# Performance work log

Measured on AMD Instinct MI355X. Metric: run time of the kernel, lower is better.

## Reference

```python
import jax, jax.numpy as jnp
import numpy as np

ROUTER_TEMP = 1.0
ALPHA = 1.0
EPS = 1e-6


def _rmsnorm(x, w):
    var = jnp.mean(x * x, axis=-1, keepdims=True)
    return x * jax.lax.rsqrt(var + EPS) * w


def _block(x, wg, wu, wd, nw):
    # stand-in recursion block: residual RMSNorm + SwiGLU MLP (pointwise over tokens)
    xn = _rmsnorm(x, nw)
    return x + (jax.nn.silu(xn @ wg) * (xn @ wu)) @ wd


def setup_inputs() -> dict:
    key = jax.random.key(0)
    ks = jax.random.split(key, 5)
    B, S, D, F, L = 2, 4096, 2048, 8192, 2
    return {
        "hidden_states": jax.random.normal(ks[0], (B, S, D), jnp.float32),
        "router_w": jax.random.normal(ks[1], (L, D), jnp.float32) * 0.02,
        "Wg": jax.random.normal(ks[2], (L, D, F), jnp.float32) * (D ** -0.5),
        "Wu": jax.random.normal(ks[3], (L, D, F), jnp.float32) * (D ** -0.5),
        "Wd": jax.random.normal(ks[4], (L, F, D), jnp.float32) * (F ** -0.5),
        "norm_w": jnp.ones((L, D), jnp.float32),
    }


def reference(hidden_states, router_w, Wg, Wu, Wd, norm_w):
    L = router_w.shape[0]
    # router: logits (B,S,L), softmax probs scaled by alpha, top-1 routing
    router_logits = (hidden_states / ROUTER_TEMP) @ router_w.T
    router_probs = jax.nn.softmax(router_logits, axis=-1) * ALPHA
    idx = jnp.argmax(router_probs, axis=-1)                      # (B,S)
    weights = jnp.take_along_axis(router_probs, idx[..., None], axis=-1)  # (B,S,1)
    # run every level's block densely on all tokens (pointwise blocks =>
    # identical math to original gather/pad/compute/scatter), then select
    y = jax.vmap(_block, in_axes=(None, 0, 0, 0, 0))(hidden_states, Wg, Wu, Wd, norm_w)  # (L,B,S,D)
    onehot = jax.nn.one_hot(idx, L, dtype=hidden_states.dtype)   # (B,S,L)
    sel = jnp.einsum("lbsd,bsl->bsd", y, onehot)
    output = hidden_states + weights * sel                       # gating == 'weighted'
    # router z-loss: mean of squared logsumexp over levels
    z = jax.nn.logsumexp(router_logits, axis=-1)
    router_z_loss = jnp.mean(z * z)
    return output, router_z_loss
```

## Files before the change

kernel.cpp:

```cpp
#include <hip/hip_runtime.h>
#include <hip/hip_bf16.h>
#include <stdint.h>

#define B_    2
#define S_    4096
#define D_    2048
#define F_    8192
#define L_    2
#define FQ    (F_ / 4)
#define NTOK  (B_ * S_)
#define RCAP  (NTOK + 128)
#define EPS_  1e-6f

typedef __attribute__((ext_vector_type(8))) short s16x8;
typedef __attribute__((ext_vector_type(4))) float f32x4;

typedef unsigned short u16;
typedef unsigned int   u32;

#define OFF_CNT   ((size_t)0)
#define OFF_ZL    ((size_t)128)
#define OFF_MAP   ((size_t)384)
#define OFF_WROW  ((size_t)33664)
#define OFF_WTOK  ((size_t)66944)
#define OFF_XG    ((size_t)99712)
#define OFF_HQ    ((size_t)34178432)
#define OFF_WA    ((size_t)68257152)
#define OFF_WB    ((size_t)85034368)

__device__ __forceinline__ u16 f2bf(float f) {
    u32 u = __builtin_bit_cast(u32, f);
    u += 0x7fff + ((u >> 16) & 1);
    return (u16)(u >> 16);
}

__device__ __forceinline__ void gl16(const u16* g, u16* l) {
    __builtin_amdgcn_global_load_lds(
        (const __attribute__((address_space(1))) void*)g,
        (__attribute__((address_space(3))) void*)l, 16, 0, 0);
}

__global__ void k_init(int* counts, float* zacc) {
    if (threadIdx.x == 0) { counts[0] = 0; counts[16] = 0; }
    zacc[threadIdx.x & 63] = 0.f;
}

__global__ __launch_bounds__(256) void k_router(
    const float* __restrict__ hs, const float* __restrict__ rw,
    const float* __restrict__ nw, int* __restrict__ counts,
    float* __restrict__ zacc, int* __restrict__ tmap,
    float* __restrict__ wrow, float* __restrict__ wtok, u16* __restrict__ Xg)
{
    int t = blockIdx.x;
    int tid = threadIdx.x;
    const float* x = hs + (size_t)t * D_;
    float xs[8];
    float sxx = 0.f, s0 = 0.f, s1 = 0.f;
#pragma unroll
    for (int i = 0; i < 8; i++) {
        int d = tid + i * 256;
        float v = x[d];
        xs[i] = v;
        sxx += v * v;
        s0  += v * rw[d];
        s1  += v * rw[D_ + d];
    }
#pragma unroll
    for (int off = 32; off; off >>= 1) {
        sxx += __shfl_down(sxx, off, 64);
        s0  += __shfl_down(s0,  off, 64);
        s1  += __shfl_down(s1,  off, 64);
    }
    __shared__ float red[3][4];
    __shared__ float bcf[1];
    __shared__ int   bci[2];
    int wave = tid >> 6, lane = tid & 63;
    if (lane == 0) { red[0][wave] = sxx; red[1][wave] = s0; red[2][wave] = s1; }
    __syncthreads();
    if (tid == 0) {
        sxx = red[0][0] + red[0][1] + red[0][2] + red[0][3];
        s0  = red[1][0] + red[1][1] + red[1][2] + red[1][3];
        s1  = red[2][0] + red[2][1] + red[2][2] + red[2][3];
        float m  = fmaxf(s0, s1);
        float e0 = __expf(s0 - m), e1 = __expf(s1 - m);
        float Z  = e0 + e1;
        int   idx = (s1 > s0) ? 1 : 0;
        float p   = ((idx == 0) ? e0 : e1) / Z;
        float z   = m + __logf(Z);
        atomicAdd(&zacc[t & 63], z * z * (1.0f / NTOK));
        int pos = atomicAdd(&counts[idx << 4], 1);
        int row = (idx == 0) ? pos : (RCAP - 1 - pos);
        tmap[row] = t;
        wrow[row] = p;
        wtok[t]   = p;
        bcf[0] = rsqrtf(sxx * (1.0f / D_) + EPS_);
        bci[0] = idx; bci[1] = row;
    }
    __syncthreads();
    float inv = bcf[0];
    int idx = bci[0], row = bci[1];
    u16* xr = Xg + (size_t)row * D_;
    const float* w = nw + (size_t)idx * D_;
#pragma unroll
    for (int i = 0; i < 8; i++) {
        int d = tid + i * 256;
        xr[d] = f2bf(xs[i] * inv * w[d]);
    }
}

__global__ __launch_bounds__(256) void k_gap(const int* counts, int* tmap, u16* Xg) {
    int row = counts[0] + blockIdx.x;
    uint4* p = (uint4*)(Xg + (size_t)row * D_);
    p[threadIdx.x] = make_uint4(0u, 0u, 0u, 0u);
    if (threadIdx.x == 0) tmap[row] = -1;
}

__global__ __launch_bounds__(256) void k_outinit(
    const float* __restrict__ hs, const float* __restrict__ wtok,
    float* __restrict__ out)
{
    int t = blockIdx.x;
    float c = 1.f + wtok[t];
    const float4* ip = (const float4*)(hs + (size_t)t * D_);
    float4* op = (float4*)(out + (size_t)t * D_);
#pragma unroll
    for (int i = 0; i < 2; i++) {
        float4 v = ip[threadIdx.x + i * 256];
        v.x *= c; v.y *= c; v.z *= c; v.w *= c;
        op[threadIdx.x + i * 256] = v;
    }
}

__global__ __launch_bounds__(256) void k_transpose(
    const float* __restrict__ in, u16* __restrict__ out,
    int R, int C, int r0, int c0, int RL, int CL)
{
    __shared__ float tile[32][33];
    int lc0 = blockIdx.x * 32;
    int lr0 = blockIdx.y * 32;
    const float* ip = in + (size_t)blockIdx.z * (size_t)R * (size_t)C;
    u16* op = out + (size_t)blockIdx.z * (size_t)CL * (size_t)RL;
    int tx = threadIdx.x & 31, ty = threadIdx.x >> 5;
#pragma unroll
    for (int i = 0; i < 4; i++)
        tile[ty + i * 8][tx] = ip[(size_t)(r0 + lr0 + ty + i * 8) * C + (c0 + lc0 + tx)];
    __syncthreads();
#pragma unroll
    for (int i = 0; i < 4; i++)
        op[(size_t)(lc0 + ty + i * 8) * RL + lr0 + tx] = f2bf(tile[tx][ty + i * 8]);
}

__global__ __launch_bounds__(256, 2) void k_gemm1(
    const u16* __restrict__ Xg, const u16* __restrict__ WgT,
    const u16* __restrict__ WuT, const int* __restrict__ counts,
    u16* __restrict__ Hq)
{
    int nt = blockIdx.x, mt = blockIdx.y;
    int count0 = counts[0];
    int level = (mt * 128 < count0) ? 0 : 1;
    const u16* Bg = WgT + (size_t)level * FQ * D_;
    const u16* Bu = WuT + (size_t)level * FQ * D_;

    __shared__ __align__(16) u16 As[128 * 32], Bgs[64 * 32], Bus[64 * 32];

    int tid = threadIdx.x, lane = tid & 63, wave = tid >> 6;
    int wm = wave >> 1, wn = wave & 1;
    int quad = lane >> 4, ln = lane & 15;

    f32x4 accG[4][2] = {}, accU[4][2] = {};

    const u16* ga = Xg + (size_t)(mt * 128 + (tid >> 2)) * D_ + (tid & 3) * 8;
    const u16* gg = Bg + (size_t)(nt * 64 + (tid >> 2)) * D_ + (tid & 3) * 8;
    const u16* gu = Bu + (size_t)(nt * 64 + (tid >> 2)) * D_ + (tid & 3) * 8;

    u16* lA = As  + (size_t)wave * 512;
    u16* lG = Bgs + (size_t)wave * 512;
    u16* lU = Bus + (size_t)wave * 512;

    for (int k0 = 0; k0 < D_; k0 += 32) {
        __syncthreads();
        gl16(ga + k0, lA);
        gl16(ga + (size_t)64 * D_ + k0, lA + 2048);
        gl16(gg + k0, lG);
        gl16(gu + k0, lU);
        __syncthreads();
        s16x8 a[4], bg[2], bu[2];
#pragma unroll
        for (int i = 0; i < 4; i++)
            a[i]  = *(const s16x8*)(As  + (wm * 64 + i * 16 + ln) * 32 + quad * 8);
#pragma unroll
        for (int j = 0; j < 2; j++) {
            bg[j] = *(const s16x8*)(Bgs + (wn * 32 + j * 16 + ln) * 32 + quad * 8);
            bu[j] = *(const s16x8*)(Bus + (wn * 32 + j * 16 + ln) * 32 + quad * 8);
        }
#pragma unroll
        for (int mi = 0; mi < 4; mi++)
#pragma unroll
            for (int ni = 0; ni < 2; ni++) {
                accG[mi][ni] = __builtin_amdgcn_mfma_f32_16x16x32_bf16(a[mi], bg[ni], accG[mi][ni], 0, 0, 0);
                accU[mi][ni] = __builtin_amdgcn_mfma_f32_16x16x32_bf16(a[mi], bu[ni], accU[mi][ni], 0, 0, 0);
            }
    }

    int rowbase = mt * 128 + wm * 64;
    int colbase = nt * 64 + wn * 32;
#pragma unroll
    for (int mi = 0; mi < 4; mi++)
#pragma unroll
        for (int ni = 0; ni < 2; ni++)
#pragma unroll
            for (int r = 0; r < 4; r++) {
                float g = accG[mi][ni][r], u = accU[mi][ni][r];
                float h = g / (1.f + __expf(-g)) * u;
                int row = rowbase + mi * 16 + quad * 4 + r;
                int col = colbase + ni * 16 + ln;
                Hq[(size_t)row * FQ + col] = f2bf(h);
            }
}

__global__ __launch_bounds__(256, 2) void k_gemm2(
    const u16* __restrict__ Hq, const u16* __restrict__ WdT,
    const int* __restrict__ counts, const int* __restrict__ tmap,
    const float* __restrict__ wrow, float* __restrict__ out)
{
    int nt = blockIdx.x, mt = blockIdx.y;
    int count0 = counts[0];
    int level = (mt * 128 < count0) ? 0 : 1;
    const u16* Bd = WdT + (size_t)level * D_ * FQ;

    __shared__ __align__(16) u16 As[128 * 32], Bs[128 * 32];
    __shared__ int   stok[128];
    __shared__ float sw[128];

    int tid = threadIdx.x, lane = tid & 63, wave = tid >> 6;
    int wm = wave >> 1, wn = wave & 1;
    int quad = lane >> 4, ln = lane & 15;

    if (tid < 128) { stok[tid] = tmap[mt * 128 + tid]; sw[tid] = wrow[mt * 128 + tid]; }

    f32x4 acc[4][4] = {};

    const u16* ga = Hq + (size_t)(mt * 128 + (tid >> 2)) * FQ + (tid & 3) * 8;
    const u16* gb = Bd + (size_t)(nt * 128 + (tid >> 2)) * FQ + (tid & 3) * 8;

    u16* lA = As + (size_t)wave * 512;
    u16* lB = Bs + (size_t)wave * 512;

    for (int k0 = 0; k0 < FQ; k0 += 32) {
        __syncthreads();
        gl16(ga + k0, lA);
        gl16(ga + (size_t)64 * FQ + k0, lA + 2048);
        gl16(gb + k0, lB);
        gl16(gb + (size_t)64 * FQ + k0, lB + 2048);
        __syncthreads();
        s16x8 a[4], b[4];
#pragma unroll
        for (int i = 0; i < 4; i++) {
            a[i] = *(const s16x8*)(As + (wm * 64 + i * 16 + ln) * 32 + quad * 8);
            b[i] = *(const s16x8*)(Bs + (wn * 64 + i * 16 + ln) * 32 + quad * 8);
        }
#pragma unroll
        for (int mi = 0; mi < 4; mi++)
#pragma unroll
            for (int ni = 0; ni < 4; ni++)
                acc[mi][ni] = __builtin_amdgcn_mfma_f32_16x16x32_bf16(a[mi], b[ni], acc[mi][ni], 0, 0, 0);
    }

    int colbase = nt * 128 + wn * 64;
#pragma unroll
    for (int mi = 0; mi < 4; mi++)
#pragma unroll
        for (int ni = 0; ni < 4; ni++)
#pragma unroll
            for (int r = 0; r < 4; r++) {
                int rl = wm * 64 + mi * 16 + quad * 4 + r;
                int tok = stok[rl];
                if (tok < 0) continue;
                float w = sw[rl];
                int col = colbase + ni * 16 + ln;
                size_t oidx = (size_t)tok * D_ + col;
                out[oidx] += w * acc[mi][ni][r];
            }
}

__global__ void k_zout(const float* zacc, float* out) {
    float s = 0.f;
#pragma unroll
    for (int i = 0; i < 64; i++) s += zacc[i];
    out[(size_t)NTOK * D_] = s;
}

extern "C" void kernel_launch(void* const* d_in, const int* in_sizes, int n_in,
                              void* d_out, int out_size, void* d_ws, size_t ws_size,
                              hipStream_t stream) {
    const float* hs = (const float*)d_in[0];
    const float* rw = (const float*)d_in[1];
    const float* Wg = (const float*)d_in[2];
    const float* Wu = (const float*)d_in[3];
    const float* Wd = (const float*)d_in[4];
    const float* nw = (const float*)d_in[5];
    float* out = (float*)d_out;

    char* ws = (char*)d_ws;
    int*   counts = (int*)(ws + OFF_CNT);
    float* zacc   = (float*)(ws + OFF_ZL);
    int*   tmap   = (int*)(ws + OFF_MAP);
    float* wrow   = (float*)(ws + OFF_WROW);
    float* wtok   = (float*)(ws + OFF_WTOK);
    u16*   Xg     = (u16*)(ws + OFF_XG);
    u16*   Hq     = (u16*)(ws + OFF_HQ);
    u16*   WA     = (u16*)(ws + OFF_WA);
    u16*   WB     = (u16*)(ws + OFF_WB);

    k_init<<<1, 64, 0, stream>>>(counts, zacc);
    k_router<<<NTOK, 256, 0, stream>>>(hs, rw, nw, counts, zacc, tmap, wrow, wtok, Xg);
    k_gap<<<128, 256, 0, stream>>>(counts, tmap, Xg);
    k_outinit<<<NTOK, 256, 0, stream>>>(hs, wtok, out);

    for (int q = 0; q < 4; q++) {
        k_transpose<<<dim3(FQ / 32, D_ / 32, L_), 256, 0, stream>>>(Wg, WA, D_, F_, 0, q * FQ, D_, FQ);
        k_transpose<<<dim3(FQ / 32, D_ / 32, L_), 256, 0, stream>>>(Wu, WB, D_, F_, 0, q * FQ, D_, FQ);
        k_gemm1<<<dim3(FQ / 64, RCAP / 128), 256, 0, stream>>>(Xg, WA, WB, counts, Hq);
        k_transpose<<<dim3(D_ / 32, FQ / 32, L_), 256, 0, stream>>>(Wd, WA, F_, D_, q * FQ, 0, FQ, D_);
        k_gemm2<<<dim3(D_ / 128, RCAP / 128), 256, 0, stream>>>(Hq, WA, counts, tmap, wrow, out);
    }
    k_zout<<<1, 1, 0, stream>>>(zacc, out);
}
```

Before: 1.830 ms.

## Pipeline GEMMs with multi-buffered LDS, larger tiles and swizzled loads

Both GEMM kernels move to 512-thread blocks with 256-wide N tiles. Global-to-LDS loads go into a 3-stage (gemm1) or 4-stage (gemm2) ring buffer, using manual vmcnt waits and raw barriers instead of two __syncthreads per K step. An XOR swizzle on the LDS layout reduces bank conflicts, and s_setprio raises wave priority around the MFMA blocks. This is meant to hide global load latency and cut sync overhead, at the cost of much more LDS per block, which lowers occupancy, and of fragile hand-written waitcnt logic.

```diff
diff --git a/kernel.cpp b/kernel.cpp
--- a/kernel.cpp
+++ b/kernel.cpp
@@ -39,6 +39,8 @@
         (const __attribute__((address_space(1))) void*)g,
         (__attribute__((address_space(3))) void*)l, 16, 0, 0);
 }
+
+#define MF(acc, va, vb) acc = __builtin_amdgcn_mfma_f32_16x16x32_bf16(va, vb, acc, 0, 0, 0)
 
 __global__ void k_init(int* counts, float* zacc) {
     if (threadIdx.x == 0) { counts[0] = 0; counts[16] = 0; }
@@ -150,7 +152,7 @@
         op[(size_t)(lc0 + ty + i * 8) * RL + lr0 + tx] = f2bf(tile[tx][ty + i * 8]);
 }
 
-__global__ __launch_bounds__(256, 2) void k_gemm1(
+__global__ __launch_bounds__(512, 2) void k_gemm1(
     const u16* __restrict__ Xg, const u16* __restrict__ WgT,
     const u16* __restrict__ WuT, const int* __restrict__ counts,
     u16* __restrict__ Hq)
@@ -161,64 +163,115 @@
     const u16* Bg = WgT + (size_t)level * FQ * D_;
     const u16* Bu = WuT + (size_t)level * FQ * D_;
 
-    __shared__ __align__(16) u16 As[128 * 32], Bgs[64 * 32], Bus[64 * 32];
+    __shared__ __align__(16) u16 lds[3 * 20480];
 
     int tid = threadIdx.x, lane = tid & 63, wave = tid >> 6;
-    int wm = wave >> 1, wn = wave & 1;
+    int wm = wave >> 2, wn = wave & 3;
     int quad = lane >> 4, ln = lane & 15;
 
-    f32x4 accG[4][2] = {}, accU[4][2] = {};
-
-    const u16* ga = Xg + (size_t)(mt * 128 + (tid >> 2)) * D_ + (tid & 3) * 8;
-    const u16* gg = Bg + (size_t)(nt * 64 + (tid >> 2)) * D_ + (tid & 3) * 8;
-    const u16* gu = Bu + (size_t)(nt * 64 + (tid >> 2)) * D_ + (tid & 3) * 8;
-
-    u16* lA = As  + (size_t)wave * 512;
-    u16* lG = Bgs + (size_t)wave * 512;
-    u16* lU = Bus + (size_t)wave * 512;
-
-    for (int k0 = 0; k0 < D_; k0 += 32) {
-        __syncthreads();
-        gl16(ga + k0, lA);
-        gl16(ga + (size_t)64 * D_ + k0, lA + 2048);
-        gl16(gg + k0, lG);
-        gl16(gu + k0, lU);
-        __syncthreads();
+    int srow = tid >> 2;
+    int sswz = ((tid & 3) ^ (srow & 3)) * 8;
+    const u16* gA  = Xg + (size_t)(mt * 128 + srow) * D_ + sswz;
+    const u16* gG0 = Bg + (size_t)(nt * 256 + srow) * D_ + sswz;
+    const u16* gG1 = gG0 + (size_t)128 * D_;
+    const u16* gU0 = Bu + (size_t)(nt * 256 + srow) * D_ + sswz;
+    const u16* gU1 = gU0 + (size_t)128 * D_;
+
+    u16* wd = lds + wave * 512;
+
+    f32x4 accG[4][4] = {}, accU[4][4] = {};
+
+#pragma unroll
+    for (int p = 0; p < 2; ++p) {
+        u16* b = wd + p * 20480;
+        gl16(gA  + p * 32, b);
+        gl16(gG0 + p * 32, b + 4096);
+        gl16(gG1 + p * 32, b + 8192);
+        gl16(gU0 + p * 32, b + 12288);
+        gl16(gU1 + p * 32, b + 16384);
+    }
+    asm volatile("s_waitcnt vmcnt(5)" ::: "memory");
+    asm volatile("s_barrier" ::: "memory");
+
+    int fswz = (quad ^ (ln & 3)) * 8;
+    int aoff = (wm * 64 + ln) * 32 + fswz;
+    int boff = (wn * 64 + ln) * 32 + fswz;
+
+    int cur = 0;
+    for (int t = 0; t < 64; ++t) {
+        const u16* As = lds + cur * 20480;
+        const u16* Gs = As + 4096;
+        const u16* Us = As + 12288;
+        int stg = cur + 2; if (stg >= 3) stg -= 3;
+        u16* sb = lds + stg * 20480 + wave * 512;
+        int koff = (t + 2) * 32;
+        bool do_stage = (t + 2) < 64;
+
         s16x8 a[4], bg[2], bu[2];
 #pragma unroll
-        for (int i = 0; i < 4; i++)
-            a[i]  = *(const s16x8*)(As  + (wm * 64 + i * 16 + ln) * 32 + quad * 8);
-#pragma unroll
-        for (int j = 0; j < 2; j++) {
-            bg[j] = *(const s16x8*)(Bgs + (wn * 32 + j * 16 + ln) * 32 + quad * 8);
-            bu[j] = *(const s16x8*)(Bus + (wn * 32 + j * 16 + ln) * 32 + quad * 8);
-        }
-#pragma unroll
-        for (int mi = 0; mi < 4; mi++)
-#pragma unroll
-            for (int ni = 0; ni < 2; ni++) {
-                accG[mi][ni] = __builtin_amdgcn_mfma_f32_16x16x32_bf16(a[mi], bg[ni], accG[mi][ni], 0, 0, 0);
-                accU[mi][ni] = __builtin_amdgcn_mfma_f32_16x16x32_bf16(a[mi], bu[ni], accU[mi][ni], 0, 0, 0);
+        for (int i = 0; i < 4; ++i) a[i] = *(const s16x8*)(As + i * 512 + aoff);
+#pragma unroll
+        for (int j = 0; j < 2; ++j) {
+            bg[j] = *(const s16x8*)(Gs + j * 512 + boff);
+            bu[j] = *(const s16x8*)(Us + j * 512 + boff);
+        }
+        if (do_stage) {
+            gl16(gA  + koff, sb);
+            gl16(gG0 + koff, sb + 4096);
+            gl16(gG1 + koff, sb + 8192);
+        }
+        __builtin_amdgcn_s_setprio(1);
+#pragma unroll
+        for (int mi = 0; mi < 4; ++mi)
+#pragma unroll
+            for (int j = 0; j < 2; ++j) {
+                MF(accG[mi][j], a[mi], bg[j]);
+                MF(accU[mi][j], a[mi], bu[j]);
             }
+        __builtin_amdgcn_s_setprio(0);
+        asm volatile("s_barrier" ::: "memory");
+
+#pragma unroll
+        for (int j = 0; j < 2; ++j) {
+            bg[j] = *(const s16x8*)(Gs + (2 + j) * 512 + boff);
+            bu[j] = *(const s16x8*)(Us + (2 + j) * 512 + boff);
+        }
+        if (do_stage) {
+            gl16(gU0 + koff, sb + 12288);
+            gl16(gU1 + koff, sb + 16384);
+        }
+        __builtin_amdgcn_s_setprio(1);
+#pragma unroll
+        for (int mi = 0; mi < 4; ++mi)
+#pragma unroll
+            for (int j = 0; j < 2; ++j) {
+                MF(accG[mi][2 + j], a[mi], bg[j]);
+                MF(accU[mi][2 + j], a[mi], bu[j]);
+            }
+        __builtin_amdgcn_s_setprio(0);
+        if (t < 62)       { asm volatile("s_waitcnt vmcnt(5)" ::: "memory"); }
+        else if (t == 62) { asm volatile("s_waitcnt vmcnt(0)" ::: "memory"); }
+        asm volatile("s_barrier" ::: "memory");
+        cur = (cur == 2) ? 0 : cur + 1;
     }
 
     int rowbase = mt * 128 + wm * 64;
-    int colbase = nt * 64 + wn * 32;
-#pragma unroll
-    for (int mi = 0; mi < 4; mi++)
-#pragma unroll
-        for (int ni = 0; ni < 2; ni++)
-#pragma unroll
-            for (int r = 0; r < 4; r++) {
-                float g = accG[mi][ni][r], u = accU[mi][ni][r];
+    int colbase = nt * 256 + wn * 64;
+#pragma unroll
+    for (int mi = 0; mi < 4; ++mi)
+#pragma unroll
+        for (int nj = 0; nj < 4; ++nj)
+#pragma unroll
+            for (int r = 0; r < 4; ++r) {
+                float g = accG[mi][nj][r], u = accU[mi][nj][r];
                 float h = g / (1.f + __expf(-g)) * u;
                 int row = rowbase + mi * 16 + quad * 4 + r;
-                int col = colbase + ni * 16 + ln;
+                int col = colbase + nj * 16 + ln;
                 Hq[(size_t)row * FQ + col] = f2bf(h);
             }
 }
 
-__global__ __launch_bounds__(256, 2) void k_gemm2(
+__global__ __launch_bounds__(512, 2) void k_gemm2(
     const u16* __restrict__ Hq, const u16* __restrict__ WdT,
     const int* __restrict__ counts, const int* __restrict__ tmap,
     const float* __restrict__ wrow, float* __restrict__ out)
@@ -228,58 +281,85 @@
     int level = (mt * 128 < count0) ? 0 : 1;
     const u16* Bd = WdT + (size_t)level * D_ * FQ;
 
-    __shared__ __align__(16) u16 As[128 * 32], Bs[128 * 32];
+    __shared__ __align__(16) u16 lds[4 * 12288];
     __shared__ int   stok[128];
     __shared__ float sw[128];
 
     int tid = threadIdx.x, lane = tid & 63, wave = tid >> 6;
-    int wm = wave >> 1, wn = wave & 1;
+    int wm = wave >> 2, wn = wave & 3;
     int quad = lane >> 4, ln = lane & 15;
 
     if (tid < 128) { stok[tid] = tmap[mt * 128 + tid]; sw[tid] = wrow[mt * 128 + tid]; }
 
+    int srow = tid >> 2;
+    int sswz = ((tid & 3) ^ (srow & 3)) * 8;
+    const u16* gA  = Hq + (size_t)(mt * 128 + srow) * FQ + sswz;
+    const u16* gB0 = Bd + (size_t)(nt * 256 + srow) * FQ + sswz;
+    const u16* gB1 = gB0 + (size_t)128 * FQ;
+
+    u16* wd = lds + wave * 512;
+
     f32x4 acc[4][4] = {};
 
-    const u16* ga = Hq + (size_t)(mt * 128 + (tid >> 2)) * FQ + (tid & 3) * 8;
-    const u16* gb = Bd + (size_t)(nt * 128 + (tid >> 2)) * FQ + (tid & 3) * 8;
-
-    u16* lA = As + (size_t)wave * 512;
-    u16* lB = Bs + (size_t)wave * 512;
-
-    for (int k0 = 0; k0 < FQ; k0 += 32) {
-        __syncthreads();
-        gl16(ga + k0, lA);
-        gl16(ga + (size_t)64 * FQ + k0, lA + 2048);
-        gl16(gb + k0, lB);
-        gl16(gb + (size_t)64 * FQ + k0, lB + 2048);
-        __syncthreads();
+#pragma unroll
+    for (int p = 0; p < 3; ++p) {
+        u16* b = wd + p * 12288;
+        gl16(gA  + p * 32, b);
+        gl16(gB0 + p * 32, b + 4096);
+        gl16(gB1 + p * 32, b + 8192);
+    }
+    asm volatile("s_waitcnt vmcnt(6)" ::: "memory");
+    asm volatile("s_barrier" ::: "memory");
+
+    int fswz = (quad ^ (ln & 3)) * 8;
+    int aoff = (wm * 64 + ln) * 32 + fswz;
+    int boff = (wn * 64 + ln) * 32 + fswz;
+
+    int cur = 0;
+    for (int t = 0; t < 64; ++t) {
+        const u16* As = lds + cur * 12288;
+        const u16* Bs = As + 4096;
+        int stg = cur + 3; if (stg >= 4) stg -= 4;
+        u16* sb = lds + stg * 12288 + wave * 512;
+        int koff = (t + 3) * 32;
+
         s16x8 a[4], b[4];
 #pragma unroll
-        for (int i = 0; i < 4; i++) {
-            a[i] = *(const s16x8*)(As + (wm * 64 + i * 16 + ln) * 32 + quad * 8);
-            b[i] = *(const s16x8*)(Bs + (wn * 64 + i * 16 + ln) * 32 + quad * 8);
-        }
-#pragma unroll
-        for (int mi = 0; mi < 4; mi++)
-#pragma unroll
-            for (int ni = 0; ni < 4; ni++)
-                acc[mi][ni] = __builtin_amdgcn_mfma_f32_16x16x32_bf16(a[mi], b[ni], acc[mi][ni], 0, 0, 0);
-    }
-
-    int colbase = nt * 128 + wn * 64;
-#pragma unroll
-    for (int mi = 0; mi < 4; mi++)
-#pragma unroll
-        for (int ni = 0; ni < 4; ni++)
-#pragma unroll
-            for (int r = 0; r < 4; r++) {
+        for (int i = 0; i < 4; ++i) {
+            a[i] = *(const s16x8*)(As + i * 512 + aoff);
+            b[i] = *(const s16x8*)(Bs + i * 512 + boff);
+        }
+        if (t + 3 < 64) {
+            gl16(gA  + koff, sb);
+            gl16(gB0 + koff, sb + 4096);
+            gl16(gB1 + koff, sb + 8192);
+        }
+        __builtin_amdgcn_s_setprio(1);
+#pragma unroll
+        for (int mi = 0; mi < 4; ++mi)
+#pragma unroll
+            for (int nj = 0; nj < 4; ++nj)
+                MF(acc[mi][nj], a[mi], b[nj]);
+        __builtin_amdgcn_s_setprio(0);
+        if (t < 61)       { asm volatile("s_waitcnt vmcnt(6)" ::: "memory"); }
+        else if (t == 61) { asm volatile("s_waitcnt vmcnt(3)" ::: "memory"); }
+        else if (t == 62) { asm volatile("s_waitcnt vmcnt(0)" ::: "memory"); }
+        asm volatile("s_barrier" ::: "memory");
+        cur = (cur == 3) ? 0 : cur + 1;
+    }
+
+    int colbase = nt * 256 + wn * 64;
+#pragma unroll
+    for (int mi = 0; mi < 4; ++mi)
+#pragma unroll
+        for (int nj = 0; nj < 4; ++nj)
+#pragma unroll
+            for (int r = 0; r < 4; ++r) {
                 int rl = wm * 64 + mi * 16 + quad * 4 + r;
                 int tok = stok[rl];
                 if (tok < 0) continue;
-                float w = sw[rl];
-                int col = colbase + ni * 16 + ln;
-                size_t oidx = (size_t)tok * D_ + col;
-                out[oidx] += w * acc[mi][ni][r];
+                int col = colbase + nj * 16 + ln;
+                out[(size_t)tok * D_ + col] += sw[rl] * acc[mi][nj][r];
             }
 }
 
@@ -320,9 +400,9 @@
     for (int q = 0; q < 4; q++) {
         k_transpose<<<dim3(FQ / 32, D_ / 32, L_), 256, 0, stream>>>(Wg, WA, D_, F_, 0, q * FQ, D_, FQ);
         k_transpose<<<dim3(FQ / 32, D_ / 32, L_), 256, 0, stream>>>(Wu, WB, D_, F_, 0, q * FQ, D_, FQ);
-        k_gemm1<<<dim3(FQ / 64, RCAP / 128), 256, 0, stream>>>(Xg, WA, WB, counts, Hq);
+        k_gemm1<<<dim3(FQ / 256, RCAP / 128), 512, 0, stream>>>(Xg, WA, WB, counts, Hq);
         k_transpose<<<dim3(D_ / 32, FQ / 32, L_), 256, 0, stream>>>(Wd, WA, F_, D_, q * FQ, 0, FQ, D_);
-        k_gemm2<<<dim3(D_ / 128, RCAP / 128), 256, 0, stream>>>(Hq, WA, counts, tmap, wrow, out);
+        k_gemm2<<<dim3(D_ / 256, RCAP / 128), 512, 0, stream>>>(Hq, WA, counts, tmap, wrow, out);
     }
     k_zout<<<1, 1, 0, stream>>>(zacc, out);
 }
```

New measurement: 1.886 ms. 1.03x slower.

## Widen GEMM K-step to 64 with XOR-swizzled LDS and merge Wg/Wu transposes

Applied to the files above, without the earlier changes.

Both GEMM kernels now stage 64-wide K slices into LDS with an XOR swizzle on the 16-byte chunks, which halves the number of barrier pairs and is meant to avoid LDS bank conflicts on the fragment reads. gemm2 uses a smaller 128x64 output tile with fewer accumulators, and both kernels raise launch-bounds occupancy to 3 blocks. The separate Wg and Wu transposes are merged into one launch. LDS arrays are padded, apparently to limit occupancy. The narrower gemm2 tile reuses each A tile less and reads Hq more times.

```diff
diff --git a/kernel.cpp b/kernel.cpp
--- a/kernel.cpp
+++ b/kernel.cpp
@@ -39,6 +39,8 @@
         (const __attribute__((address_space(1))) void*)g,
         (__attribute__((address_space(3))) void*)l, 16, 0, 0);
 }
+
+#define MF(acc, va, vb) acc = __builtin_amdgcn_mfma_f32_16x16x32_bf16(va, vb, acc, 0, 0, 0)
 
 __global__ void k_init(int* counts, float* zacc) {
     if (threadIdx.x == 0) { counts[0] = 0; counts[16] = 0; }
@@ -131,6 +133,27 @@
     }
 }
 
+__global__ __launch_bounds__(256) void k_transposeGU(
+    const float* __restrict__ Wg, const float* __restrict__ Wu,
+    u16* __restrict__ WA, u16* __restrict__ WB, int c0)
+{
+    __shared__ float tile[32][33];
+    int z = blockIdx.z;
+    int m = z & 1, lvl = z >> 1;
+    const float* ip = (m ? Wu : Wg) + (size_t)lvl * D_ * F_;
+    u16* op = (m ? WB : WA) + (size_t)lvl * FQ * D_;
+    int lc0 = blockIdx.x * 32;
+    int lr0 = blockIdx.y * 32;
+    int tx = threadIdx.x & 31, ty = threadIdx.x >> 5;
+#pragma unroll
+    for (int i = 0; i < 4; i++)
+        tile[ty + i * 8][tx] = ip[(size_t)(lr0 + ty + i * 8) * F_ + (c0 + lc0 + tx)];
+    __syncthreads();
+#pragma unroll
+    for (int i = 0; i < 4; i++)
+        op[(size_t)(lc0 + ty + i * 8) * D_ + lr0 + tx] = f2bf(tile[tx][ty + i * 8]);
+}
+
 __global__ __launch_bounds__(256) void k_transpose(
     const float* __restrict__ in, u16* __restrict__ out,
     int R, int C, int r0, int c0, int RL, int CL)
@@ -150,7 +173,7 @@
         op[(size_t)(lc0 + ty + i * 8) * RL + lr0 + tx] = f2bf(tile[tx][ty + i * 8]);
 }
 
-__global__ __launch_bounds__(256, 2) void k_gemm1(
+__global__ __launch_bounds__(256, 3) void k_gemm1(
     const u16* __restrict__ Xg, const u16* __restrict__ WgT,
     const u16* __restrict__ WuT, const int* __restrict__ counts,
     u16* __restrict__ Hq)
@@ -161,64 +184,75 @@
     const u16* Bg = WgT + (size_t)level * FQ * D_;
     const u16* Bu = WuT + (size_t)level * FQ * D_;
 
-    __shared__ __align__(16) u16 As[128 * 32], Bgs[64 * 32], Bus[64 * 32];
+    __shared__ __align__(16) u16 As[8192 + 6144];
+    __shared__ __align__(16) u16 Gs[4096], Us[4096];
 
     int tid = threadIdx.x, lane = tid & 63, wave = tid >> 6;
     int wm = wave >> 1, wn = wave & 1;
     int quad = lane >> 4, ln = lane & 15;
+    int swz = ln & 7;
 
     f32x4 accG[4][2] = {}, accU[4][2] = {};
 
-    const u16* ga = Xg + (size_t)(mt * 128 + (tid >> 2)) * D_ + (tid & 3) * 8;
-    const u16* gg = Bg + (size_t)(nt * 64 + (tid >> 2)) * D_ + (tid & 3) * 8;
-    const u16* gu = Bu + (size_t)(nt * 64 + (tid >> 2)) * D_ + (tid & 3) * 8;
-
-    u16* lA = As  + (size_t)wave * 512;
-    u16* lG = Bgs + (size_t)wave * 512;
-    u16* lU = Bus + (size_t)wave * 512;
-
-    for (int k0 = 0; k0 < D_; k0 += 32) {
+    int srow = tid >> 3;
+    int sswz = ((tid & 7) ^ (srow & 7)) * 8;
+    const u16* gA = Xg + (size_t)(mt * 128 + srow) * D_ + sswz;
+    const u16* gG = Bg + (size_t)(nt * 64 + srow) * D_ + sswz;
+    const u16* gU = Bu + (size_t)(nt * 64 + srow) * D_ + sswz;
+    u16* dA = As + wave * 512;
+    u16* dG = Gs + wave * 512;
+    u16* dU = Us + wave * 512;
+
+    for (int k0 = 0; k0 < D_; k0 += 64) {
         __syncthreads();
-        gl16(ga + k0, lA);
-        gl16(ga + (size_t)64 * D_ + k0, lA + 2048);
-        gl16(gg + k0, lG);
-        gl16(gu + k0, lU);
+        gl16(gA + k0, dA);
+        gl16(gA + (size_t)32 * D_ + k0, dA + 2048);
+        gl16(gA + (size_t)64 * D_ + k0, dA + 4096);
+        gl16(gA + (size_t)96 * D_ + k0, dA + 6144);
+        gl16(gG + k0, dG);
+        gl16(gG + (size_t)32 * D_ + k0, dG + 2048);
+        gl16(gU + k0, dU);
+        gl16(gU + (size_t)32 * D_ + k0, dU + 2048);
         __syncthreads();
-        s16x8 a[4], bg[2], bu[2];
-#pragma unroll
-        for (int i = 0; i < 4; i++)
-            a[i]  = *(const s16x8*)(As  + (wm * 64 + i * 16 + ln) * 32 + quad * 8);
-#pragma unroll
-        for (int j = 0; j < 2; j++) {
-            bg[j] = *(const s16x8*)(Bgs + (wn * 32 + j * 16 + ln) * 32 + quad * 8);
-            bu[j] = *(const s16x8*)(Bus + (wn * 32 + j * 16 + ln) * 32 + quad * 8);
+#pragma unroll
+        for (int h = 0; h < 2; ++h) {
+            int ks = ((h * 4 + quad) ^ swz) * 8;
+            s16x8 a[4], bg[2], bu[2];
+#pragma unroll
+            for (int i = 0; i < 4; ++i)
+                a[i] = *(const s16x8*)(As + (wm * 64 + i * 16 + ln) * 64 + ks);
+#pragma unroll
+            for (int j = 0; j < 2; ++j) {
+                bg[j] = *(const s16x8*)(Gs + (wn * 32 + j * 16 + ln) * 64 + ks);
+                bu[j] = *(const s16x8*)(Us + (wn * 32 + j * 16 + ln) * 64 + ks);
+            }
+#pragma unroll
+            for (int mi = 0; mi < 4; ++mi)
+#pragma unroll
+                for (int j = 0; j < 2; ++j) {
+                    MF(accG[mi][j], a[mi], bg[j]);
+                    MF(accU[mi][j], a[mi], bu[j]);
+                }
         }
-#pragma unroll
-        for (int mi = 0; mi < 4; mi++)
-#pragma unroll
-            for (int ni = 0; ni < 2; ni++) {
-                accG[mi][ni] = __builtin_amdgcn_mfma_f32_16x16x32_bf16(a[mi], bg[ni], accG[mi][ni], 0, 0, 0);
-                accU[mi][ni] = __builtin_amdgcn_mfma_f32_16x16x32_bf16(a[mi], bu[ni], accU[mi][ni], 0, 0, 0);
-            }
     }
 
     int rowbase = mt * 128 + wm * 64;
     int colbase = nt * 64 + wn * 32;
 #pragma unroll
-    for (int mi = 0; mi < 4; mi++)
-#pragma unroll
-        for (int ni = 0; ni < 2; ni++)
-#pragma unroll
-            for (int r = 0; r < 4; r++) {
-                float g = accG[mi][ni][r], u = accU[mi][ni][r];
+    for (int mi = 0; mi < 4; ++mi)
+#pragma unroll
+        for (int j = 0; j < 2; ++j)
+#pragma unroll
+            for (int r = 0; r < 4; ++r) {
+                float g = accG[mi][j][r], u = accU[mi][j][r];
                 float h = g / (1.f + __expf(-g)) * u;
                 int row = rowbase + mi * 16 + quad * 4 + r;
-                int col = colbase + ni * 16 + ln;
+                int col = colbase + j * 16 + ln;
                 Hq[(size_t)row * FQ + col] = f2bf(h);
             }
 }
 
-__global__ __launch_bounds__(256, 2) void k_gemm2(
+__global__ __launch_bounds__(256, 3) void k_gemm2(
     const u16* __restrict__ Hq, const u16* __restrict__ WdT,
     const int* __restrict__ counts, const int* __restrict__ tmap,
     const float* __restrict__ wrow, float* __restrict__ out)
@@ -228,58 +262,66 @@
     int level = (mt * 128 < count0) ? 0 : 1;
     const u16* Bd = WdT + (size_t)level * D_ * FQ;
 
-    __shared__ __align__(16) u16 As[128 * 32], Bs[128 * 32];
+    __shared__ __align__(16) u16 As[8192 + 9728];
+    __shared__ __align__(16) u16 Bs[4096];
     __shared__ int   stok[128];
     __shared__ float sw[128];
 
     int tid = threadIdx.x, lane = tid & 63, wave = tid >> 6;
     int wm = wave >> 1, wn = wave & 1;
     int quad = lane >> 4, ln = lane & 15;
+    int swz = ln & 7;
 
     if (tid < 128) { stok[tid] = tmap[mt * 128 + tid]; sw[tid] = wrow[mt * 128 + tid]; }
 
-    f32x4 acc[4][4] = {};
-
-    const u16* ga = Hq + (size_t)(mt * 128 + (tid >> 2)) * FQ + (tid & 3) * 8;
-    const u16* gb = Bd + (size_t)(nt * 128 + (tid >> 2)) * FQ + (tid & 3) * 8;
-
-    u16* lA = As + (size_t)wave * 512;
-    u16* lB = Bs + (size_t)wave * 512;
-
-    for (int k0 = 0; k0 < FQ; k0 += 32) {
+    f32x4 acc[4][2] = {};
+
+    int srow = tid >> 3;
+    int sswz = ((tid & 7) ^ (srow & 7)) * 8;
+    const u16* gA = Hq + (size_t)(mt * 128 + srow) * FQ + sswz;
+    const u16* gB = Bd + (size_t)(nt * 64 + srow) * FQ + sswz;
+    u16* dA = As + wave * 512;
+    u16* dB = Bs + wave * 512;
+
+    for (int k0 = 0; k0 < FQ; k0 += 64) {
         __syncthreads();
-        gl16(ga + k0, lA);
-        gl16(ga + (size_t)64 * FQ + k0, lA + 2048);
-        gl16(gb + k0, lB);
-        gl16(gb + (size_t)64 * FQ + k0, lB + 2048);
+        gl16(gA + k0, dA);
+        gl16(gA + (size_t)32 * FQ + k0, dA + 2048);
+        gl16(gA + (size_t)64 * FQ + k0, dA + 4096);
+        gl16(gA + (size_t)96 * FQ + k0, dA + 6144);
+        gl16(gB + k0, dB);
+        gl16(gB + (size_t)32 * FQ + k0, dB + 2048);
         __syncthreads();
-        s16x8 a[4], b[4];
-#pragma unroll
-        for (int i = 0; i < 4; i++) {
-            a[i] = *(const s16x8*)(As + (wm * 64 + i * 16 + ln) * 32 + quad * 8);
-            b[i] = *(const s16x8*)(Bs + (wn * 64 + i * 16 + ln) * 32 + quad * 8);
+#pragma unroll
+        for (int h = 0; h < 2; ++h) {
+            int ks = ((h * 4 + quad) ^ swz) * 8;
+            s16x8 a[4], b[2];
+#pragma unroll
+            for (int i = 0; i < 4; ++i)
+                a[i] = *(const s16x8*)(As + (wm * 64 + i * 16 + ln) * 64 + ks);
+#pragma unroll
+            for (int j = 0; j < 2; ++j)
+                b[j] = *(const s16x8*)(Bs + (wn * 32 + j * 16 + ln) * 64 + ks);
+#pragma unroll
+            for (int mi = 0; mi < 4; ++mi)
+#pragma unroll
+                for (int j = 0; j < 2; ++j)
+                    MF(acc[mi][j], a[mi], b[j]);
         }
-#pragma unroll
-        for (int mi = 0; mi < 4; mi++)
-#pragma unroll
-            for (int ni = 0; ni < 4; ni++)
-                acc[mi][ni] = __builtin_amdgcn_mfma_f32_16x16x32_bf16(a[mi], b[ni], acc[mi][ni], 0, 0, 0);
-    }
-
-    int colbase = nt * 128 + wn * 64;
-#pragma unroll
-    for (int mi = 0; mi < 4; mi++)
-#pragma unroll
-        for (int ni = 0; ni < 4; ni++)
-#pragma unroll
-            for (int r = 0; r < 4; r++) {
+    }
+
+    int colbase = nt * 64 + wn * 32;
+#pragma unroll
+    for (int mi = 0; mi < 4; ++mi)
+#pragma unroll
+        for (int j = 0; j < 2; ++j)
+#pragma unroll
+            for (int r = 0; r < 4; ++r) {
                 int rl = wm * 64 + mi * 16 + quad * 4 + r;
                 int tok = stok[rl];
                 if (tok < 0) continue;
-                float w = sw[rl];
-                int col = colbase + ni * 16 + ln;
-                size_t oidx = (size_t)tok * D_ + col;
-                out[oidx] += w * acc[mi][ni][r];
+                int col = colbase + j * 16 + ln;
+                out[(size_t)tok * D_ + col] += sw[rl] * acc[mi][j][r];
             }
 }
 
@@ -318,11 +360,10 @@
     k_outinit<<<NTOK, 256, 0, stream>>>(hs, wtok, out);
 
     for (int q = 0; q < 4; q++) {
-        k_transpose<<<dim3(FQ / 32, D_ / 32, L_), 256, 0, stream>>>(Wg, WA, D_, F_, 0, q * FQ, D_, FQ);
-        k_transpose<<<dim3(FQ / 32, D_ / 32, L_), 256, 0, stream>>>(Wu, WB, D_, F_, 0, q * FQ, D_, FQ);
+        k_transposeGU<<<dim3(FQ / 32, D_ / 32, 2 * L_), 256, 0, stream>>>(Wg, Wu, WA, WB, q * FQ);
         k_gemm1<<<dim3(FQ / 64, RCAP / 128), 256, 0, stream>>>(Xg, WA, WB, counts, Hq);
         k_transpose<<<dim3(D_ / 32, FQ / 32, L_), 256, 0, stream>>>(Wd, WA, F_, D_, q * FQ, 0, FQ, D_);
-        k_gemm2<<<dim3(D_ / 128, RCAP / 128), 256, 0, stream>>>(Hq, WA, counts, tmap, wrow, out);
+        k_gemm2<<<dim3(D_ / 64, RCAP / 128), 256, 0, stream>>>(Hq, WA, counts, tmap, wrow, out);
     }
     k_zout<<<1, 1, 0, stream>>>(zacc, out);
 }
```

After: 1.561 ms. -14.7%, faster.
